# Kernel optimization log

Hardware: AMD Instinct MI355X
Metric: run time of the kernel (lower is better)

The kernel has to match this reference:

```python
import jax, jax.numpy as jnp
import numpy as np
from jax import lax

B, D_DATA, D_LAT = 1024, 16384, 256
N_GRID = 256  # silhouette integration grid
EPS = 1e-12


def pairwise_dist(z):
    # z: [n, d] -> Euclidean distance matrix [n, n]
    sq = jnp.sum(z * z, axis=-1)
    d2 = sq[:, None] + sq[None, :] - 2.0 * (z @ z.T)
    return jnp.sqrt(jnp.clip(d2, 0.0) + EPS)


def mst_deaths(dist):
    # H0 persistence of Vietoris-Rips from a distance matrix: births are 0,
    # deaths are the MST edge weights (single-linkage merge heights).
    # Prim's algorithm, vectorized per step, scanned n-1 times.
    n = dist.shape[0]
    in_tree = jnp.zeros((n,), dtype=bool).at[0].set(True)
    mindist = dist[0]

    def step(carry, _):
        in_tree, mindist = carry
        cand = jnp.where(in_tree, jnp.inf, mindist)
        j = jnp.argmin(cand)
        w = cand[j]
        in_tree = in_tree.at[j].set(True)
        mindist = jnp.minimum(mindist, dist[j])
        return (in_tree, mindist), w

    _, deaths = lax.scan(step, (in_tree, mindist), None, length=n - 1)
    return deaths  # [n-1] persistences (births = 0)


def silhouette_value(deaths):
    # Power-1 persistence silhouette phi(t) = sum_j w_j L_j(t) / sum_j w_j,
    # L_j(t) = max(0, min(t - b_j, d_j - t)) with b_j = 0; scalar = mean over grid.
    w = deaths  # persistence^1 weights
    tmax = lax.stop_gradient(jnp.max(deaths))
    t = jnp.linspace(0.0, 1.0, N_GRID) * tmax  # [T]
    tent = jnp.maximum(0.0, jnp.minimum(t[None, :], deaths[:, None] - t[None, :]))
    phi = (w[:, None] * tent).sum(0) / (w.sum() + EPS)
    return jnp.mean(phi)


def setup_inputs() -> dict:
    key = jax.random.key(0)
    k1, k2, k3, k4, k5 = jax.random.split(key, 5)
    return {
        "recon_x": jax.random.normal(k1, (B, D_DATA), dtype=jnp.float32),
        "x": jax.random.normal(k2, (B, D_DATA), dtype=jnp.float32),
        "mu": jax.random.normal(k3, (B, D_LAT), dtype=jnp.float32),
        "logvar": jax.random.normal(k4, (B, D_LAT), dtype=jnp.float32),
        "representations": jax.random.normal(k5, (B, D_LAT), dtype=jnp.float32),
    }


def reference(recon_x, x, mu, logvar, representations):
    recon_weight, kl_weight, topo_weight = 1.0, 0.1, 0.5
    reg_weight = 1.0  # TopologicalRegularization(weight=1.0)

    recon_loss = jnp.mean((recon_x - x) ** 2)
    kl_loss = -0.5 * jnp.mean(1.0 + logvar - mu * mu - jnp.exp(logvar))

    dist = pairwise_dist(representations)
    deaths = mst_deaths(dist)          # dim-0 diagram persistences
    topo_loss = reg_weight * silhouette_value(deaths)

    total = recon_weight * recon_loss + kl_weight * kl_loss + topo_weight * topo_loss
    return total, recon_loss, kl_loss, topo_loss
```

## Files before the change

### kernel.cpp

```cpp
#include <hip/hip_runtime.h>
#include <hip/hip_bf16.h>
#include <math.h>


#define NBLK 1024
#define PBLK 64

__device__ __forceinline__ float sub2(const float4 a, const float4 b) {
  const float dx = a.x - b.x, dy = a.y - b.y, dz = a.z - b.z, dw = a.w - b.w;
  return dx * dx + dy * dy + dz * dz + dw * dw;
}

__global__ __launch_bounds__(512) void losses_kernel(const float4* __restrict__ rx,
                                                     const float4* __restrict__ x,
                                                     const float4* __restrict__ mu,
                                                     const float4* __restrict__ lv,
                                                     const float* __restrict__ z,
                                                     float* __restrict__ partials,
                                                     float* __restrict__ sq,
                                                     unsigned long long* __restrict__ cmin01) {
  const int t = threadIdx.x;
  const int b = blockIdx.x;
  if (b == 0) {
    for (int v = t; v < 2048; v += 512) cmin01[v] = ~0ull;
  }
  const int base = b * 4096 + t;
  float rs = 0.f;
#pragma unroll
  for (int k = 0; k < 2; ++k) {
    const int i0 = base + k * 2048;
    const float4 a0 = rx[i0],        c0 = x[i0];
    const float4 a1 = rx[i0 + 512],  c1 = x[i0 + 512];
    const float4 a2 = rx[i0 + 1024], c2 = x[i0 + 1024];
    const float4 a3 = rx[i0 + 1536], c3 = x[i0 + 1536];
    rs += sub2(a0, c0) + sub2(a1, c1) + sub2(a2, c2) + sub2(a3, c3);
  }
  float ks = 0.f;
  const int gid = b * 512 + t;
  if (gid < 65536) {
    const float4 m = mu[gid], l = lv[gid];
    ks += 1.f + l.x - m.x * m.x - __expf(l.x);
    ks += 1.f + l.y - m.y * m.y - __expf(l.y);
    ks += 1.f + l.z - m.z * m.z - __expf(l.z);
    ks += 1.f + l.w - m.w * m.w - __expf(l.w);
  }
#pragma unroll
  for (int off = 32; off; off >>= 1) {
    rs += __shfl_xor(rs, off);
    ks += __shfl_xor(ks, off);
  }
  __shared__ float red[16];
  if ((t & 63) == 0) { red[t >> 6] = rs; red[8 + (t >> 6)] = ks; }
  __syncthreads();
  if (t == 0) {
    float a = 0.f, c = 0.f;
#pragma unroll
    for (int w = 0; w < 8; ++w) { a += red[w]; c += red[8 + w]; }
    partials[b] = a;
    partials[NBLK + b] = c;
  }
  if (b < 128) {
    const int lane = t & 63;
    const int row = b * 8 + (t >> 6);
    const float4 v = ((const float4*)(z + row * 256))[lane];
    float s = v.x * v.x + v.y * v.y + v.z * v.z + v.w * v.w;
#pragma unroll
    for (int off = 32; off; off >>= 1) s += __shfl_xor(s, off);
    if (lane == 0) sq[row] = s;
  }
}

__global__ __launch_bounds__(256) void dist_kernel(const float* __restrict__ z,
                                                   const float* __restrict__ sq,
                                                   float* __restrict__ dist,
                                                   unsigned long long* __restrict__ cmin0) {
  __shared__ float A[64][68];
  __shared__ float Bs[64][68];
  const int i0 = (blockIdx.x >> 4) * 64, j0 = (blockIdx.x & 15) * 64;
  const int t = threadIdx.x;
  const int tx = t & 15;
  const int ty = t >> 4;
  float acc[4][4] = {};
  for (int k0 = 0; k0 < 256; k0 += 64) {
    __syncthreads();
#pragma unroll
    for (int it = 0; it < 4; ++it) {
      int lin = it * 256 + t;
      int row = lin >> 4, q = lin & 15;
      *(float4*)&A[row][q * 4]  = *(const float4*)(z + (i0 + row) * 256 + k0 + q * 4);
      *(float4*)&Bs[row][q * 4] = *(const float4*)(z + (j0 + row) * 256 + k0 + q * 4);
    }
    __syncthreads();
#pragma unroll 4
    for (int k = 0; k < 64; k += 4) {
      float4 av[4], bv[4];
#pragma unroll
      for (int rr = 0; rr < 4; ++rr) av[rr] = *(const float4*)&A[ty + 16 * rr][k];
#pragma unroll
      for (int cc = 0; cc < 4; ++cc) bv[cc] = *(const float4*)&Bs[tx + 16 * cc][k];
#pragma unroll
      for (int rr = 0; rr < 4; ++rr)
#pragma unroll
        for (int cc = 0; cc < 4; ++cc) {
          acc[rr][cc] += av[rr].x * bv[cc].x;
          acc[rr][cc] += av[rr].y * bv[cc].y;
          acc[rr][cc] += av[rr].z * bv[cc].z;
          acc[rr][cc] += av[rr].w * bv[cc].w;
        }
    }
  }
  unsigned long long rowbest[4] = {~0ull, ~0ull, ~0ull, ~0ull};
#pragma unroll
  for (int rr = 0; rr < 4; ++rr) {
    const int i = i0 + ty + 16 * rr;
    const float sqi = sq[i];
#pragma unroll
    for (int cc = 0; cc < 4; ++cc) {
      const int j = j0 + tx + 16 * cc;
      const float d2 = sqi + sq[j] - 2.f * acc[rr][cc];
      const float d = sqrtf(fmaxf(d2, 0.f) + 1e-12f);
      dist[i * 1024 + j] = (j == i) ? 0.f : d;
      if (j != i) {
        const int lo = i < j ? i : j;
        const int hi = i + j - lo;
        const unsigned long long key =
            ((unsigned long long)__float_as_uint(d) << 32)
          | (unsigned long long)((lo << 10) | hi);
        if (key < rowbest[rr]) rowbest[rr] = key;
      }
    }
  }
#pragma unroll
  for (int rr = 0; rr < 4; ++rr) {
    unsigned long long best = rowbest[rr];
#pragma unroll
    for (int off = 8; off; off >>= 1) {
      const unsigned int blo = __shfl_xor((unsigned int)best, off);
      const unsigned int bhi = __shfl_xor((unsigned int)(best >> 32), off);
      const unsigned long long o = ((unsigned long long)bhi << 32) | blo;
      if (o < best) best = o;
    }
    if (tx == 0) {
      unsigned long long* p = &cmin0[i0 + ty + 16 * rr];
      const unsigned long long cur =
          __hip_atomic_load(p, __ATOMIC_RELAXED, __HIP_MEMORY_SCOPE_AGENT);
      if (best < cur) atomicMin(p, best);
    }
  }
}

__device__ __forceinline__ int phase_b_dev(const unsigned long long* __restrict__ cbuf,
                                           int* scomp, unsigned long long* cl,
                                           int* pnew, int* sred,
                                           bool record, float* sdeaths, int* scnt) {
  const int t = threadIdx.x;
  for (int v = t; v < 1024; v += 256)
    cl[v] = __hip_atomic_load(&cbuf[v], __ATOMIC_RELAXED, __HIP_MEMORY_SCOPE_AGENT);
  if (t == 0) sred[0] = 0;
  __syncthreads();
  for (int v = t; v < 1024; v += 256) {
    int parent = scomp[v];
    if (parent == v) {
      const unsigned long long key = cl[v];
      if (key != ~0ull) {
        const int lo = (int)((key >> 10) & 1023), hi = (int)(key & 1023);
        const int clo = scomp[lo], chi = scomp[hi];
        const int other = (clo == v) ? chi : clo;
        const bool mutual = (cl[other] == key);
        if (record && (!mutual || v < other)) {
          const int pos = atomicAdd(scnt, 1);
          sdeaths[pos] = __uint_as_float((unsigned int)(key >> 32));
        }
        parent = (mutual && v < other) ? v : other;
      }
    }
    pnew[v] = parent;
  }
  __syncthreads();
#pragma unroll
  for (int it = 0; it < 2; ++it) {
    int q0 = pnew[pnew[t]];
    int q1 = pnew[pnew[t + 256]];
    int q2 = pnew[pnew[t + 512]];
    int q3 = pnew[pnew[t + 768]];
    __syncthreads();
    pnew[t] = q0; pnew[t + 256] = q1; pnew[t + 512] = q2; pnew[t + 768] = q3;
    __syncthreads();
  }
  int nroots = 0;
#pragma unroll
  for (int q = 0; q < 4; ++q) {
    const int v = t + q * 256;
    int p = pnew[v];
    while (p != pnew[p]) p = pnew[p];
    scomp[v] = p;
    if (p == v) ++nroots;
  }
  atomicAdd(&sred[0], nroots);
  __syncthreads();
  return sred[0];
}

__global__ __launch_bounds__(256) void mst_kernel(const float* __restrict__ dist,
                                                  unsigned long long* __restrict__ cminb,
                                                  const float* __restrict__ partials,
                                                  float* __restrict__ out) {
  __shared__ int scomp[1024];
  __shared__ int pnew[1024];
  __shared__ unsigned long long cl[1024];
  __shared__ float sdeaths[1023];
  __shared__ int sred[2];
  __shared__ float redf[12];
  const int t = threadIdx.x;
  const int b = blockIdx.x;
  const bool rec = (b == 0);

  for (int v = t; v < 1024; v += 256) scomp[v] = v;
  if (t == 0) sred[1] = 0;
  if (t < 16)
    __hip_atomic_store(&cminb[2048 + b * 16 + t], ~0ull,
                       __ATOMIC_RELAXED, __HIP_MEMORY_SCOPE_AGENT);
  __syncthreads();

  int ncomp = phase_b_dev(cminb, scomp, cl, pnew, sred, rec, sdeaths, &sred[1]);

  const int lane = t & 63;
  const int w = t >> 6;
  for (int r = 1; r < 10 && ncomp > 1; ++r) {
    unsigned long long* cbuf = cminb + (r % 3) * 1024;
#pragma unroll
    for (int q = 0; q < 4; ++q) {
      const int i = b * 16 + w * 4 + q;
      const int ci = scomp[i];
      const float* row = dist + i * 1024;
      unsigned long long best = ~0ull;
#pragma unroll
      for (int k = 0; k < 4; ++k) {
        const int j0 = lane * 4 + k * 256;
        const float4 d4 = *(const float4*)(row + j0);
        const int4 c4 = *(const int4*)(&scomp[j0]);
        const float dv[4] = {d4.x, d4.y, d4.z, d4.w};
        const int cv[4] = {c4.x, c4.y, c4.z, c4.w};
#pragma unroll
        for (int c = 0; c < 4; ++c) {
          if (cv[c] != ci) {
            const int j = j0 + c;
            const int lo = i < j ? i : j;
            const int hi = i + j - lo;
            const unsigned long long key =
                ((unsigned long long)__float_as_uint(dv[c]) << 32)
              | (unsigned long long)((lo << 10) | hi);
            if (key < best) best = key;
          }
        }
      }
#pragma unroll
      for (int off = 32; off; off >>= 1) {
        const unsigned int blo = __shfl_xor((unsigned int)best, off);
        const unsigned int bhi = __shfl_xor((unsigned int)(best >> 32), off);
        const unsigned long long o = ((unsigned long long)bhi << 32) | blo;
        if (o < best) best = o;
      }
      if (lane == 0 && best != ~0ull) {
        const unsigned long long cur =
            __hip_atomic_load(&cbuf[ci], __ATOMIC_RELAXED, __HIP_MEMORY_SCOPE_AGENT);
        if (best < cur) atomicMin(&cbuf[ci], best);
      }
    }
    int* ctrp = (int*)(dist + (size_t)r * 1025);
    __syncthreads();
    if (t == 0) {
      __hip_atomic_fetch_add(ctrp, 1, __ATOMIC_ACQ_REL, __HIP_MEMORY_SCOPE_AGENT);
      while (__hip_atomic_load(ctrp, __ATOMIC_ACQUIRE, __HIP_MEMORY_SCOPE_AGENT) < PBLK)
        __builtin_amdgcn_s_sleep(2);
    }
    __syncthreads();
    if (t < 16)
      __hip_atomic_store(&cminb[((r - 1) % 3) * 1024 + b * 16 + t], ~0ull,
                         __ATOMIC_RELAXED, __HIP_MEMORY_SCOPE_AGENT);
    ncomp = phase_b_dev(cbuf, scomp, cl, pnew, sred, rec, sdeaths, &sred[1]);
  }

  if (b != 0) return;
  float lmax = 0.f, lsum = 0.f;
  for (int v = t; v < 1023; v += 256) {
    const float d = sdeaths[v];
    lmax = fmaxf(lmax, d);
    lsum += d;
  }
#pragma unroll
  for (int off = 32; off; off >>= 1) {
    lmax = fmaxf(lmax, __shfl_xor(lmax, off));
    lsum += __shfl_xor(lsum, off);
  }
  if ((t & 63) == 0) { redf[t >> 6] = lmax; redf[4 + (t >> 6)] = lsum; }
  __syncthreads();
  const float tmax = fmaxf(fmaxf(redf[0], redf[1]), fmaxf(redf[2], redf[3]));
  const float wsum = redf[4] + redf[5] + redf[6] + redf[7];
  const float tt = (float)t * (1.0f / 255.0f) * tmax;
  float acc = 0.f;
  for (int j = 0; j < 1023; ++j) {
    const float dj = sdeaths[j];
    acc += dj * fmaxf(fminf(tt, dj - tt), 0.f);
  }
  float phi = acc / (wsum + 1e-12f);
  float rs = 0.f, ks = 0.f;
  for (int v = t; v < 1024; v += 256) { rs += partials[v]; ks += partials[1024 + v]; }
#pragma unroll
  for (int off = 32; off; off >>= 1) {
    phi += __shfl_xor(phi, off);
    rs += __shfl_xor(rs, off);
    ks += __shfl_xor(ks, off);
  }
  __syncthreads();
  if ((t & 63) == 0) { redf[t >> 6] = phi; redf[4 + (t >> 6)] = rs; redf[8 + (t >> 6)] = ks; }
  __syncthreads();
  if (t == 0) {
    const float topo = (redf[0] + redf[1] + redf[2] + redf[3]) * (1.f / 256.f);
    const float recon = (redf[4] + redf[5] + redf[6] + redf[7]) * (1.f / 16777216.f);
    const float kl = -0.5f * (redf[8] + redf[9] + redf[10] + redf[11]) * (1.f / 262144.f);
    const float total = recon + 0.1f * kl + 0.5f * topo;
    out[0] = (float)__float2bfloat16(total);
    out[1] = (float)__float2bfloat16(recon);
    out[2] = (float)__float2bfloat16(kl);
    out[3] = (float)__float2bfloat16(topo);
  }
}

extern "C" void kernel_launch(void* const* d_in, const int* in_sizes, int n_in,
                              void* d_out, int out_size, void* d_ws, size_t ws_size,
                              hipStream_t stream) {
  const float* rx = (const float*)d_in[0];
  const float* x  = (const float*)d_in[1];
  const float* mu = (const float*)d_in[2];
  const float* lv = (const float*)d_in[3];
  const float* z  = (const float*)d_in[4];

  float* wsf = (float*)d_ws;
  unsigned long long* cminb = (unsigned long long*)wsf;
  float* sq       = wsf + 4096;
  float* partials = wsf + 6144;
  float* dist     = wsf + 8192;
  float* out      = (float*)d_out;

  losses_kernel<<<NBLK, 512, 0, stream>>>((const float4*)rx, (const float4*)x,
                                          (const float4*)mu, (const float4*)lv,
                                          z, partials, sq, cminb);
  dist_kernel<<<256, 256, 0, stream>>>(z, sq, dist, cminb);
  mst_kernel<<<PBLK, 256, 0, stream>>>(dist, cminb, partials, out);
}
```

Baseline: 229.9 us.

## Finish MST with contracted component graph and single-block Prim once components are few

Boruvka rounds now stop once the component count drops to 100 or fewer, instead of running until one component remains. The remaining components are relabeled with a prefix sum, and every block builds a min-edge matrix between components in shared memory. These matrices are merged into a global matrix with atomics, and block 0 then runs a wavefront Prim over the small component graph. The aim is to replace several grid-wide Boruvka rounds and their barriers with one contraction pass plus a cheap serial finish. The cost is an extra full pass over the distance rows, two more grid barriers, and scratch space taken from inside the dist buffer.

New measurement: 262.9 us. 1.14x slower.

```diff
diff --git a/kernel.cpp b/kernel.cpp
--- a/kernel.cpp
+++ b/kernel.cpp
@@ -5,6 +5,7 @@
 
 #define NBLK 1024
 #define PBLK 64
+#define CMAX 100
 
 __device__ __forceinline__ float sub2(const float4 a, const float4 b) {
   const float dx = a.x - b.x, dy = a.y - b.y, dz = a.z - b.z, dw = a.w - b.w;
@@ -201,13 +202,14 @@
   return sred[0];
 }
 
-__global__ __launch_bounds__(256) void mst_kernel(const float* __restrict__ dist,
+__global__ __launch_bounds__(256) void mst_kernel(float* __restrict__ dist,
                                                   unsigned long long* __restrict__ cminb,
                                                   const float* __restrict__ partials,
                                                   float* __restrict__ out) {
   __shared__ int scomp[1024];
   __shared__ int pnew[1024];
   __shared__ unsigned long long cl[1024];
+  __shared__ unsigned int cmat[CMAX * CMAX];
   __shared__ float sdeaths[1023];
   __shared__ int sred[2];
   __shared__ float redf[12];
@@ -226,7 +228,7 @@
 
   const int lane = t & 63;
   const int w = t >> 6;
-  for (int r = 1; r < 10 && ncomp > 1; ++r) {
+  for (int r = 1; r < 10 && ncomp > CMAX; ++r) {
     unsigned long long* cbuf = cminb + (r % 3) * 1024;
 #pragma unroll
     for (int q = 0; q < 4; ++q) {
@@ -281,7 +283,121 @@
     ncomp = phase_b_dev(cbuf, scomp, cl, pnew, sred, rec, sdeaths, &sred[1]);
   }
 
-  if (b != 0) return;
+  unsigned int* gcm = (unsigned int*)(dist + 1008 * 1024);
+  int* flag = (int*)(dist + (size_t)10 * 1025);
+  int* wbar = (int*)(dist + (size_t)11 * 1025);
+
+  if (ncomp > 1) {
+    const int c = ncomp;
+    int* itmp = (int*)cl;
+    for (int v = t; v < 1024; v += 256) itmp[v] = (scomp[v] == v) ? 1 : 0;
+    __syncthreads();
+    for (int off = 1; off < 1024; off <<= 1) {
+      int vals[4];
+#pragma unroll
+      for (int q = 0; q < 4; ++q) {
+        const int v = t + q * 256;
+        vals[q] = itmp[v] + ((v >= off) ? itmp[v - off] : 0);
+      }
+      __syncthreads();
+#pragma unroll
+      for (int q = 0; q < 4; ++q) itmp[t + q * 256] = vals[q];
+      __syncthreads();
+    }
+    for (int v = t; v < 1024; v += 256) pnew[v] = itmp[scomp[v]] - 1;
+    for (int e = t; e < c * c; e += 256) cmat[e] = ~0u;
+    __syncthreads();
+#pragma unroll
+    for (int q = 0; q < 4; ++q) {
+      const int i = b * 16 + w * 4 + q;
+      const int a = pnew[i];
+      const float* row = dist + i * 1024;
+#pragma unroll
+      for (int k = 0; k < 4; ++k) {
+        const int j0 = lane * 4 + k * 256;
+        const float4 d4 = *(const float4*)(row + j0);
+        const int4 c4 = *(const int4*)(&pnew[j0]);
+        const float dv[4] = {d4.x, d4.y, d4.z, d4.w};
+        const int cv[4] = {c4.x, c4.y, c4.z, c4.w};
+#pragma unroll
+        for (int cc = 0; cc < 4; ++cc) {
+          if (cv[cc] != a) {
+            const unsigned int u = __float_as_uint(dv[cc]);
+            const int idx = a * c + cv[cc];
+            if (u < cmat[idx]) atomicMin(&cmat[idx], u);
+          }
+        }
+      }
+    }
+    __syncthreads();
+    if (b == PBLK - 1) {
+      for (int e = t; e < c * c; e += 256) gcm[e] = ~0u;
+      __syncthreads();
+      __threadfence();
+      if (t == 0)
+        __hip_atomic_store(flag, 1, __ATOMIC_RELEASE, __HIP_MEMORY_SCOPE_AGENT);
+    }
+    if (t == 0) {
+      while (__hip_atomic_load(flag, __ATOMIC_ACQUIRE, __HIP_MEMORY_SCOPE_AGENT) == 0)
+        __builtin_amdgcn_s_sleep(1);
+    }
+    __syncthreads();
+    for (int e = t; e < c * c; e += 256) {
+      const unsigned int u = cmat[e];
+      if (u != ~0u) {
+        const unsigned int cur =
+            __hip_atomic_load(&gcm[e], __ATOMIC_RELAXED, __HIP_MEMORY_SCOPE_AGENT);
+        if (u < cur) atomicMin(&gcm[e], u);
+      }
+    }
+    __threadfence();
+    __syncthreads();
+    if (t == 0) {
+      __hip_atomic_fetch_add(wbar, 1, __ATOMIC_ACQ_REL, __HIP_MEMORY_SCOPE_AGENT);
+      while (__hip_atomic_load(wbar, __ATOMIC_ACQUIRE, __HIP_MEMORY_SCOPE_AGENT) < PBLK)
+        __builtin_amdgcn_s_sleep(1);
+    }
+    __syncthreads();
+    if (b != 0) return;
+    for (int e = t; e < c * c; e += 256) cmat[e] = gcm[e];
+    __syncthreads();
+    const int base = sred[1];
+    if (t < 64) {
+      const int e0 = lane, e1 = 64 + lane;
+      unsigned int md0 = (e0 < c && e0 != 0) ? cmat[e0] : ~0u;
+      unsigned int md1 = (e1 < c) ? cmat[e1] : ~0u;
+      for (int step = 0; step < c - 1; ++step) {
+        unsigned long long k0 = ((unsigned long long)md0 << 32) | (unsigned int)e0;
+        unsigned long long k1 = (e1 < c) ? (((unsigned long long)md1 << 32) | (unsigned int)e1)
+                                         : ~0ull;
+        unsigned long long best = k0 < k1 ? k0 : k1;
+#pragma unroll
+        for (int off = 32; off; off >>= 1) {
+          const unsigned int blo = __shfl_xor((unsigned int)best, off);
+          const unsigned int bhi = __shfl_xor((unsigned int)(best >> 32), off);
+          const unsigned long long o = ((unsigned long long)bhi << 32) | blo;
+          if (o < best) best = o;
+        }
+        const unsigned int wb = (unsigned int)(best >> 32);
+        const int bc = (int)(best & 0xffffffffu);
+        if (lane == 0) sdeaths[base + step] = __uint_as_float(wb);
+        if (e0 == bc) md0 = ~0u;
+        if (e1 == bc) md1 = ~0u;
+        if (e0 < c && md0 != ~0u) {
+          const unsigned int nv = cmat[bc * c + e0];
+          if (nv < md0) md0 = nv;
+        }
+        if (e1 < c && md1 != ~0u) {
+          const unsigned int nv = cmat[bc * c + e1];
+          if (nv < md1) md1 = nv;
+        }
+      }
+    }
+    __syncthreads();
+  } else if (b != 0) {
+    return;
+  }
+
   float lmax = 0.f, lsum = 0.f;
   for (int v = t; v < 1023; v += 256) {
     const float d = sdeaths[v];
```
